# Kernel tuning notes

Measured on AMD Instinct MI355X. Metric: run time of the kernel, lower is better.

Reference implementation:

```python
import jax, jax.numpy as jnp
import numpy as np

SIGMA = 1.0

def setup_inputs() -> dict:
    key = jax.random.key(0)
    k1, k2 = jax.random.split(key)
    z = jax.random.normal(k1, (8192, 1024), dtype=jnp.float32)
    expert_keys = jax.random.normal(k2, (4096, 1024), dtype=jnp.float32)
    return {"z": z, "expert_keys": expert_keys}

def reference(z, expert_keys):
    # squared euclidean distances [N, E] = |z|^2 + |e|^2 - 2 z.e
    z_sq = jnp.sum(z * z, axis=-1, keepdims=True)          # [N, 1]
    e_sq = jnp.sum(expert_keys * expert_keys, axis=-1)     # [E]
    dist2 = z_sq + e_sq[None, :] - 2.0 * (z @ expert_keys.T)
    dist2 = jnp.maximum(dist2, 0.0)
    similarity = jnp.exp(-dist2 / (2.0 * SIGMA ** 2))       # [N, E]
    weights = jax.nn.softmax(similarity, axis=-1)            # [N, E]
    weighted_expert = weights @ expert_keys                  # [N, D]
    return (similarity, weighted_expert)
```

## Files before the change

kernel.cpp:

```cpp
#include <hip/hip_runtime.h>
#include <stdint.h>


#define M_TOK 8192
#define N_EXP 4096
#define D_DIM 1024

typedef __attribute__((ext_vector_type(4))) float f32x4;
typedef __attribute__((ext_vector_type(8))) short short8;
typedef unsigned short u16;
typedef unsigned int u32;

__device__ __forceinline__ u16 f32_to_bf16(float f) {
  u32 u = __builtin_bit_cast(u32, f);
  u += 0x7fff + ((u >> 16) & 1);
  return (u16)(u >> 16);
}

__device__ __forceinline__ void async16(const void* g, void* l) {
  __builtin_amdgcn_global_load_lds((__attribute__((address_space(1))) void*)(g),
                                   (__attribute__((address_space(3))) void*)(l),
                                   16, 0, 0);
}

__global__ __launch_bounds__(256) void prep_convert2(const float* __restrict__ zsrc,
                                                     const float* __restrict__ esrc,
                                                     u16* __restrict__ zdst,
                                                     u16* __restrict__ edst,
                                                     float* __restrict__ zsq,
                                                     float* __restrict__ esq) {
  int row = blockIdx.x;
  const float* src;
  u16* dst;
  float* sq;
  if (row < M_TOK) {
    src = zsrc + (size_t)row * D_DIM;
    dst = zdst + (size_t)row * D_DIM;
    sq = zsq + row;
  } else {
    int r = row - M_TOK;
    src = esrc + (size_t)r * D_DIM;
    dst = edst + (size_t)r * D_DIM;
    sq = esq + r;
  }
  int t = threadIdx.x;
  const float4 v = ((const float4*)src)[t];
  ushort4 h;
  h.x = f32_to_bf16(v.x); h.y = f32_to_bf16(v.y);
  h.z = f32_to_bf16(v.z); h.w = f32_to_bf16(v.w);
  ((ushort4*)dst)[t] = h;
  float p = v.x * v.x + v.y * v.y + v.z * v.z + v.w * v.w;
#pragma unroll
  for (int off = 1; off < 64; off <<= 1) p += __shfl_xor(p, off, 64);
  __shared__ float partial[4];
  if ((t & 63) == 0) partial[t >> 6] = p;
  __syncthreads();
  if (t == 0) *sq = partial[0] + partial[1] + partial[2] + partial[3];
}

__global__ __launch_bounds__(256) void transpose_bf16(const u16* __restrict__ src,
                                                      u16* __restrict__ dst) {
  __shared__ u16 tile[64][65];
  int e0 = blockIdx.x * 64;
  int d0 = blockIdx.y * 64;
  int t = threadIdx.x;
  int lr = t >> 4;
  int lc = (t & 15) * 4;
#pragma unroll
  for (int r8 = 0; r8 < 4; ++r8) {
    int row = lr + r8 * 16;
    ushort4 v = *(const ushort4*)(src + (size_t)(e0 + row) * D_DIM + d0 + lc);
    tile[row][lc + 0] = v.x; tile[row][lc + 1] = v.y;
    tile[row][lc + 2] = v.z; tile[row][lc + 3] = v.w;
  }
  __syncthreads();
#pragma unroll
  for (int r8 = 0; r8 < 4; ++r8) {
    int dl = lr + r8 * 16;
    ushort4 v;
    v.x = tile[lc + 0][dl]; v.y = tile[lc + 1][dl];
    v.z = tile[lc + 2][dl]; v.w = tile[lc + 3][dl];
    *(ushort4*)(dst + (size_t)(d0 + dl) * N_EXP + e0 + lc) = v;
  }
}

template <int EPI>
__global__ __launch_bounds__(256) void gemm_bt(const u16* __restrict__ A,
                                               const u16* __restrict__ Bt,
                                               int Mdim, int Ndim, int Kdim,
                                               float* __restrict__ out, int ldo,
                                               const float* __restrict__ a_sq,
                                               const float* __restrict__ b_sq,
                                               float* __restrict__ rowsum,
                                               u16* __restrict__ wb,
                                               const float* __restrict__ scale) {
  constexpr int BM = 128, BN = 128, BK = 64;
  __shared__ __align__(16) u16 smA[2 * BM * BK];
  __shared__ __align__(16) u16 smB[2 * BN * BK];

  const int nTilesN = Ndim / BN;
  const int nwg = (Mdim / BM) * nTilesN;
  const int cpx = nwg >> 3;
  const int wg = blockIdx.x;
  const int swz = (wg & 7) * cpx + (wg >> 3);
  const int m0 = (swz / nTilesN) * BM;
  const int n0 = (swz % nTilesN) * BN;

  const int t = threadIdx.x;
  const int l = t & 63;
  const int w = t >> 6;
  const int wr = w >> 1, wc = w & 1;

  const int lr8 = l >> 3;
  const int cswz = (((l & 7) ^ lr8) << 3);

  f32x4 acc[4][4];
#pragma unroll
  for (int i = 0; i < 4; ++i)
#pragma unroll
    for (int j = 0; j < 4; ++j) acc[i][j] = (f32x4){0.f, 0.f, 0.f, 0.f};

  const int nIter = Kdim / BK;

#pragma unroll
  for (int i = 0; i < 4; ++i) {
    int s = i * 4 + w;
    int row = s * 8 + lr8;
    async16(A + (size_t)(m0 + row) * Kdim + cswz, smA + s * 512);
    async16(Bt + (size_t)(n0 + row) * Kdim + cswz, smB + s * 512);
  }
  __syncthreads();

  int cur = 0;
  for (int it = 0; it < nIter; ++it) {
    if (it + 1 < nIter) {
      const int k0 = (it + 1) * BK;
      const int nb = (cur ^ 1) * 8192;
#pragma unroll
      for (int i = 0; i < 4; ++i) {
        int s = i * 4 + w;
        int row = s * 8 + lr8;
        async16(A + (size_t)(m0 + row) * Kdim + k0 + cswz, smA + nb + s * 512);
        async16(Bt + (size_t)(n0 + row) * Kdim + k0 + cswz, smB + nb + s * 512);
      }
    }

    const int cbase = cur * 8192;
#pragma unroll
    for (int ks = 0; ks < 2; ++ks) {
      short8 af[4], bf[4];
      const int lrow = l & 15;
      const int kb = ks * 64 + ((l >> 4) << 4);
#pragma unroll
      for (int mi = 0; mi < 4; ++mi) {
        int row = wr * 64 + mi * 16 + lrow;
        int addr = row * 128 + (kb ^ ((row & 7) << 4));
        af[mi] = *(const short8*)(smA + cbase + (addr >> 1));
      }
#pragma unroll
      for (int ni = 0; ni < 4; ++ni) {
        int row = wc * 64 + ni * 16 + lrow;
        int addr = row * 128 + (kb ^ ((row & 7) << 4));
        bf[ni] = *(const short8*)(smB + cbase + (addr >> 1));
      }
#pragma unroll
      for (int mi = 0; mi < 4; ++mi)
#pragma unroll
        for (int ni = 0; ni < 4; ++ni)
          acc[mi][ni] = __builtin_amdgcn_mfma_f32_16x16x32_bf16(
              bf[ni], af[mi], acc[mi][ni], 0, 0, 0);
    }

    __syncthreads();
    cur ^= 1;
  }

  const int lcol = l & 15;
  const int rgrp = l >> 4;
  if (EPI == 1) {
#pragma unroll
    for (int mi = 0; mi < 4; ++mi) {
      int grow = m0 + wr * 64 + mi * 16 + lcol;
      float zq = a_sq[grow];
      float esum = 0.f;
#pragma unroll
      for (int ni = 0; ni < 4; ++ni) {
        int ncol = n0 + wc * 64 + ni * 16 + rgrp * 4;
        f32x4 eqv = *(const f32x4*)(b_sq + ncol);
        f32x4 simv;
        ushort4 wv;
#pragma unroll
        for (int r = 0; r < 4; ++r) {
          float dist2 = fmaxf(zq + eqv[r] - 2.0f * acc[mi][ni][r], 0.0f);
          float sim = __expf(-0.5f * dist2);
          simv[r] = sim;
          float es = __expf(sim);
          (&wv.x)[r] = f32_to_bf16(es);
          esum += es;
        }
        *(f32x4*)(out + (size_t)grow * ldo + ncol) = simv;
        if (wb) *(ushort4*)(wb + (size_t)grow * ldo + ncol) = wv;
      }
      esum += __shfl_xor(esum, 16, 64);
      esum += __shfl_xor(esum, 32, 64);
      if (rgrp == 0) atomicAdd(&rowsum[grow], esum);
    }
  } else {
#pragma unroll
    for (int mi = 0; mi < 4; ++mi) {
      int grow = m0 + wr * 64 + mi * 16 + lcol;
      float s = scale ? (1.0f / scale[grow]) : 1.0f;
#pragma unroll
      for (int ni = 0; ni < 4; ++ni) {
        int ncol = n0 + wc * 64 + ni * 16 + rgrp * 4;
        f32x4 v = acc[mi][ni] * s;
        *(f32x4*)(out + (size_t)grow * ldo + ncol) = v;
      }
    }
  }
}

__global__ __launch_bounds__(256) void weights_kernel(const float* __restrict__ sim,
                                                      const float* __restrict__ rowsum,
                                                      u16* __restrict__ wb) {
  size_t i = ((size_t)blockIdx.x * 256 + threadIdx.x) * 8;
  int row = (int)(i >> 12);
  float inv = 1.0f / rowsum[row];
  float4 a = *(const float4*)(sim + i);
  float4 b = *(const float4*)(sim + i + 4);
  u32 w0 = (u32)f32_to_bf16(__expf(a.x) * inv) | ((u32)f32_to_bf16(__expf(a.y) * inv) << 16);
  u32 w1 = (u32)f32_to_bf16(__expf(a.z) * inv) | ((u32)f32_to_bf16(__expf(a.w) * inv) << 16);
  u32 w2 = (u32)f32_to_bf16(__expf(b.x) * inv) | ((u32)f32_to_bf16(__expf(b.y) * inv) << 16);
  u32 w3 = (u32)f32_to_bf16(__expf(b.z) * inv) | ((u32)f32_to_bf16(__expf(b.w) * inv) << 16);
  uint4 o; o.x = w0; o.y = w1; o.z = w2; o.w = w3;
  *(uint4*)(wb + i) = o;
}

extern "C" void kernel_launch(void* const* d_in, const int* in_sizes, int n_in,
                              void* d_out, int out_size, void* d_ws, size_t ws_size,
                              hipStream_t stream) {
  const float* z = (const float*)d_in[0];
  const float* e = (const float*)d_in[1];
  float* out = (float*)d_out;
  float* sim = out;
  float* wout = out + (size_t)M_TOK * N_EXP;

  char* ws = (char*)d_ws;
  const size_t MB = (size_t)1 << 20;
  const bool fused = ws_size >= 96 * MB + 80 * 1024;

  if (fused) {
    u16* zb  = (u16*)ws;
    u16* eb  = (u16*)(ws + 16 * MB);
    u16* ebT = (u16*)(ws + 24 * MB);
    u16* Wb  = (u16*)(ws + 32 * MB);
    float* z_sq   = (float*)(ws + 96 * MB);
    float* e_sq   = (float*)(ws + 96 * MB + 32768);
    float* rowsum = (float*)(ws + 96 * MB + 49152);

    prep_convert2<<<M_TOK + N_EXP, 256, 0, stream>>>(z, e, zb, eb, z_sq, e_sq);
    transpose_bf16<<<dim3(N_EXP / 64, D_DIM / 64), 256, 0, stream>>>(eb, ebT);
    (void)hipMemsetAsync(rowsum, 0, M_TOK * sizeof(float), stream);

    gemm_bt<1><<<(M_TOK / 128) * (N_EXP / 128), 256, 0, stream>>>(
        zb, eb, M_TOK, N_EXP, D_DIM, sim, N_EXP, z_sq, e_sq, rowsum, Wb, nullptr);

    gemm_bt<0><<<(M_TOK / 128) * (D_DIM / 128), 256, 0, stream>>>(
        Wb, ebT, M_TOK, D_DIM, N_EXP, wout, D_DIM, nullptr, nullptr, nullptr,
        nullptr, rowsum);
  } else {
    u16* Wb  = (u16*)ws;
    u16* zb  = (u16*)ws;
    u16* eb  = (u16*)(ws + 64 * MB);
    u16* ebT = (u16*)(ws + 72 * MB);
    float* z_sq   = (float*)(ws + 80 * MB);
    float* e_sq   = (float*)(ws + 80 * MB + 32768);
    float* rowsum = (float*)(ws + 80 * MB + 49152);

    prep_convert2<<<M_TOK + N_EXP, 256, 0, stream>>>(z, e, zb, eb, z_sq, e_sq);
    transpose_bf16<<<dim3(N_EXP / 64, D_DIM / 64), 256, 0, stream>>>(eb, ebT);
    (void)hipMemsetAsync(rowsum, 0, M_TOK * sizeof(float), stream);

    gemm_bt<1><<<(M_TOK / 128) * (N_EXP / 128), 256, 0, stream>>>(
        zb, eb, M_TOK, N_EXP, D_DIM, sim, N_EXP, z_sq, e_sq, rowsum, nullptr, nullptr);

    weights_kernel<<<(M_TOK * (size_t)N_EXP) / (8 * 256), 256, 0, stream>>>(sim, rowsum, Wb);

    gemm_bt<0><<<(M_TOK / 128) * (D_DIM / 128), 256, 0, stream>>>(
        Wb, ebT, M_TOK, D_DIM, N_EXP, wout, D_DIM, nullptr, nullptr, nullptr,
        nullptr, nullptr);
  }
}
```

Baseline: 201.1 us.

## Replace similarity GEMM with 256x256-tile 8-wave pipelined kernel

Adds a new kernel for the distance/similarity GEMM that uses 256x256 tiles and 512 threads (8 waves). It interleaves LDS fragment loads, async global-to-LDS staging and MFMA quarters, separated by explicit barriers, waitcnts and setprio. The goal is more data reuse per tile and global load latency hidden behind MFMA work. The cost is higher register and LDS pressure (128KB LDS per block) and fewer workgroups (512) to spread across CUs. Only the fused workspace path is switched; the fallback path keeps the old kernel.

```diff
diff --git a/kernel.cpp b/kernel.cpp
--- a/kernel.cpp
+++ b/kernel.cpp
@@ -84,6 +84,175 @@
   }
 }
 
+__device__ __forceinline__ short8 lds_frag(const u16* base, int rh, int kbyte) {
+  int ab = rh * 128 + (kbyte ^ ((rh & 7) << 4));
+  return *(const short8*)((const char*)base + ab);
+}
+
+template <int MOFF, int NOFF>
+__device__ __forceinline__ void mfma_q(f32x4 (&acc)[8][4], short8 (&af)[4][2],
+                                       short8 (&bf)[4][2]) {
+#pragma unroll
+  for (int mi = 0; mi < 4; ++mi)
+#pragma unroll
+    for (int ni = 0; ni < 2; ++ni)
+#pragma unroll
+      for (int ks = 0; ks < 2; ++ks)
+        acc[MOFF + mi][NOFF + ni] = __builtin_amdgcn_mfma_f32_16x16x32_bf16(
+            bf[NOFF + ni][ks], af[mi][ks], acc[MOFF + mi][NOFF + ni], 0, 0, 0);
+}
+
+#define BAR() __builtin_amdgcn_s_barrier()
+#define WAIT_LGKM0() do { asm volatile("s_waitcnt lgkmcnt(0)" ::: "memory"); \
+                          __builtin_amdgcn_sched_barrier(0); } while (0)
+#define WAIT_VM(n) do { asm volatile("s_waitcnt vmcnt(" #n ")" ::: "memory"); \
+                        __builtin_amdgcn_sched_barrier(0); } while (0)
+
+__global__ __launch_bounds__(512, 2) void gemm8_sim(const u16* __restrict__ A,
+                                                    const u16* __restrict__ Bt,
+                                                    int Mdim, int Ndim, int Kdim,
+                                                    float* __restrict__ out, int ldo,
+                                                    const float* __restrict__ a_sq,
+                                                    const float* __restrict__ b_sq,
+                                                    float* __restrict__ rowsum,
+                                                    u16* __restrict__ wb) {
+  constexpr int BM = 256, BN = 256, BK = 64;
+  __shared__ __align__(16) u16 smA[2][2][8192];
+  __shared__ __align__(16) u16 smB[2][2][8192];
+
+  const int nTilesN = Ndim / BN;
+  const int nwg = (Mdim / BM) * nTilesN;
+  const int cpx = nwg >> 3;
+  const int wg = blockIdx.x;
+  const int swzb = (wg & 7) * cpx + (wg >> 3);
+  const int m0 = (swzb / nTilesN) * BM;
+  const int n0 = (swzb % nTilesN) * BN;
+
+  const int t = threadIdx.x;
+  const int l = t & 63;
+  const int wid = t >> 6;
+  const int wr = wid >> 2;
+  const int wc = wid & 3;
+  const int lrow = l & 15;
+  const int kb16 = (l >> 4) << 4;
+  const int lr8 = l >> 3;
+  const int cswz = ((l & 7) ^ lr8) << 3;
+  const int st_r0 = wid * 16 + lr8;
+  const int st_r1 = wid * 16 + 8 + lr8;
+  const int bhalf = wc >> 1;
+  const int brow0 = (wc & 1) * 64;
+
+#define STAGE_A8(bufp, half, kelem) do { \
+    async16(A + (size_t)(m0 + (half)*128 + st_r0) * Kdim + (kelem) + cswz, \
+            &smA[bufp][half][(wid*2 + 0) * 512]); \
+    async16(A + (size_t)(m0 + (half)*128 + st_r1) * Kdim + (kelem) + cswz, \
+            &smA[bufp][half][(wid*2 + 1) * 512]); } while (0)
+#define STAGE_B8(bufp, half, kelem) do { \
+    async16(Bt + (size_t)(n0 + (half)*128 + st_r0) * Kdim + (kelem) + cswz, \
+            &smB[bufp][half][(wid*2 + 0) * 512]); \
+    async16(Bt + (size_t)(n0 + (half)*128 + st_r1) * Kdim + (kelem) + cswz, \
+            &smB[bufp][half][(wid*2 + 1) * 512]); } while (0)
+
+  f32x4 acc[8][4];
+#pragma unroll
+  for (int i = 0; i < 8; ++i)
+#pragma unroll
+    for (int j = 0; j < 4; ++j) acc[i][j] = (f32x4){0.f, 0.f, 0.f, 0.f};
+
+  short8 af[4][2], bf[4][2];
+
+  STAGE_A8(0, 0, 0); STAGE_A8(0, 1, 0);
+  STAGE_B8(0, 0, 0); STAGE_B8(0, 1, 0);
+  STAGE_B8(1, 0, BK); STAGE_B8(1, 1, BK);
+  WAIT_VM(4);
+  BAR();
+
+#define DO_TILE8(u_, buf_, doA_, doB_, VMN_) do { \
+     \
+    _Pragma("unroll") for (int mi = 0; mi < 4; ++mi) { \
+      af[mi][0] = lds_frag(&smA[buf_][wr][0], mi*16 + lrow, kb16); \
+      af[mi][1] = lds_frag(&smA[buf_][wr][0], mi*16 + lrow, 64 + kb16); } \
+    _Pragma("unroll") for (int ni = 0; ni < 2; ++ni) { \
+      bf[ni][0] = lds_frag(&smB[buf_][bhalf][0], brow0 + ni*16 + lrow, kb16); \
+      bf[ni][1] = lds_frag(&smB[buf_][bhalf][0], brow0 + ni*16 + lrow, 64 + kb16); } \
+    if (doA_) STAGE_A8((buf_) ^ 1, 0, ((u_) + 1) * BK); \
+    BAR(); WAIT_LGKM0(); \
+    __builtin_amdgcn_s_setprio(1); \
+    mfma_q<0, 0>(acc, af, bf); \
+    __builtin_amdgcn_s_setprio(0); \
+    BAR(); \
+     \
+    _Pragma("unroll") for (int ni = 2; ni < 4; ++ni) { \
+      bf[ni][0] = lds_frag(&smB[buf_][bhalf][0], brow0 + ni*16 + lrow, kb16); \
+      bf[ni][1] = lds_frag(&smB[buf_][bhalf][0], brow0 + ni*16 + lrow, 64 + kb16); } \
+    if (doA_) STAGE_A8((buf_) ^ 1, 1, ((u_) + 1) * BK); \
+    BAR(); WAIT_LGKM0(); \
+    __builtin_amdgcn_s_setprio(1); \
+    mfma_q<0, 2>(acc, af, bf); \
+    __builtin_amdgcn_s_setprio(0); \
+    BAR(); \
+     \
+    _Pragma("unroll") for (int mi = 0; mi < 4; ++mi) { \
+      af[mi][0] = lds_frag(&smA[buf_][wr][0], (mi+4)*16 + lrow, kb16); \
+      af[mi][1] = lds_frag(&smA[buf_][wr][0], (mi+4)*16 + lrow, 64 + kb16); } \
+    if (doB_) STAGE_B8(buf_, 0, ((u_) + 2) * BK); \
+    BAR(); WAIT_LGKM0(); \
+    __builtin_amdgcn_s_setprio(1); \
+    mfma_q<4, 0>(acc, af, bf); \
+    __builtin_amdgcn_s_setprio(0); \
+    BAR(); \
+     \
+    if (doB_) STAGE_B8(buf_, 1, ((u_) + 2) * BK); \
+    BAR(); \
+    __builtin_amdgcn_s_setprio(1); \
+    mfma_q<4, 2>(acc, af, bf); \
+    __builtin_amdgcn_s_setprio(0); \
+    WAIT_VM(VMN_); \
+    BAR(); \
+  } while (0)
+
+  const int T = Kdim / BK;
+  for (int it = 0; it < T / 2 - 1; ++it) {
+    const int u0 = 2 * it;
+    DO_TILE8(u0, 0, true, true, 4);
+    DO_TILE8(u0 + 1, 1, true, true, 4);
+  }
+  DO_TILE8(T - 2, 0, true, false, 0);
+  DO_TILE8(T - 1, 1, false, false, 0);
+
+  const int rgrp = l >> 4;
+#pragma unroll
+  for (int mi = 0; mi < 8; ++mi) {
+    int grow = m0 + wr * 128 + mi * 16 + lrow;
+    float zq = a_sq[grow];
+    float esum = 0.f;
+#pragma unroll
+    for (int ni = 0; ni < 4; ++ni) {
+      int ncol = n0 + wc * 64 + ni * 16 + rgrp * 4;
+      f32x4 eqv = *(const f32x4*)(b_sq + ncol);
+      f32x4 simv;
+      ushort4 wv;
+#pragma unroll
+      for (int r = 0; r < 4; ++r) {
+        float dist2 = fmaxf(zq + eqv[r] - 2.0f * acc[mi][ni][r], 0.0f);
+        float sim = __expf(-0.5f * dist2);
+        simv[r] = sim;
+        float es = __expf(sim);
+        (&wv.x)[r] = f32_to_bf16(es);
+        esum += es;
+      }
+      *(f32x4*)(out + (size_t)grow * ldo + ncol) = simv;
+      *(ushort4*)(wb + (size_t)grow * ldo + ncol) = wv;
+    }
+    esum += __shfl_xor(esum, 16, 64);
+    esum += __shfl_xor(esum, 32, 64);
+    if (rgrp == 0) atomicAdd(&rowsum[grow], esum);
+  }
+#undef DO_TILE8
+#undef STAGE_A8
+#undef STAGE_B8
+}
+
 template <int EPI>
 __global__ __launch_bounds__(256) void gemm_bt(const u16* __restrict__ A,
                                                const u16* __restrict__ Bt,
@@ -110,7 +279,6 @@
   const int l = t & 63;
   const int w = t >> 6;
   const int wr = w >> 1, wc = w & 1;
-
   const int lr8 = l >> 3;
   const int cswz = (((l & 7) ^ lr8) << 3);
 
@@ -121,7 +289,6 @@
     for (int j = 0; j < 4; ++j) acc[i][j] = (f32x4){0.f, 0.f, 0.f, 0.f};
 
   const int nIter = Kdim / BK;
-
 #pragma unroll
   for (int i = 0; i < 4; ++i) {
     int s = i * 4 + w;
@@ -144,7 +311,6 @@
         async16(Bt + (size_t)(n0 + row) * Kdim + k0 + cswz, smB + nb + s * 512);
       }
     }
-
     const int cbase = cur * 8192;
 #pragma unroll
     for (int ks = 0; ks < 2; ++ks) {
@@ -170,7 +336,6 @@
           acc[mi][ni] = __builtin_amdgcn_mfma_f32_16x16x32_bf16(
               bf[ni], af[mi], acc[mi][ni], 0, 0, 0);
     }
-
     __syncthreads();
     cur ^= 1;
   }
@@ -262,8 +427,8 @@
     transpose_bf16<<<dim3(N_EXP / 64, D_DIM / 64), 256, 0, stream>>>(eb, ebT);
     (void)hipMemsetAsync(rowsum, 0, M_TOK * sizeof(float), stream);
 
-    gemm_bt<1><<<(M_TOK / 128) * (N_EXP / 128), 256, 0, stream>>>(
-        zb, eb, M_TOK, N_EXP, D_DIM, sim, N_EXP, z_sq, e_sq, rowsum, Wb, nullptr);
+    gemm8_sim<<<(M_TOK / 256) * (N_EXP / 256), 512, 0, stream>>>(
+        zb, eb, M_TOK, N_EXP, D_DIM, sim, N_EXP, z_sq, e_sq, rowsum, Wb);
 
     gemm_bt<0><<<(M_TOK / 128) * (D_DIM / 128), 256, 0, stream>>>(
         Wb, ebT, M_TOK, D_DIM, N_EXP, wout, D_DIM, nullptr, nullptr, nullptr,
```

Measured after the change: 191.2 us. 4.9% less time.

## Use 8-wave GEMM blocks and an LDS-transposed epilogue with coalesced row stores

Applied to the files above, without the earlier changes.

Each 128x128 GEMM block now runs 512 threads in a 2x4 wave grid, so each wave computes a 64x32 sub-tile. That halves the per-wave accumulators, and each thread issues fewer async global-to-LDS copies per stage. The intent is to raise the number of resident waves and hide latency better. In the similarity GEMM epilogue, results are staged through LDS so that each group of 8 lanes writes contiguous row segments. Those writes use nontemporal stores for the similarity output, plus the bf16 exp weights and per-row partial sums. The costs are reloading A fragments from LDS across more waves and issuing more rowsum atomics per row.

```diff
diff --git a/kernel.cpp b/kernel.cpp
--- a/kernel.cpp
+++ b/kernel.cpp
@@ -8,6 +8,7 @@
 
 typedef __attribute__((ext_vector_type(4))) float f32x4;
 typedef __attribute__((ext_vector_type(8))) short short8;
+typedef __attribute__((ext_vector_type(4))) unsigned short u16x4;
 typedef unsigned short u16;
 typedef unsigned int u32;
 
@@ -85,15 +86,15 @@
 }
 
 template <int EPI>
-__global__ __launch_bounds__(256) void gemm_bt(const u16* __restrict__ A,
-                                               const u16* __restrict__ Bt,
-                                               int Mdim, int Ndim, int Kdim,
-                                               float* __restrict__ out, int ldo,
-                                               const float* __restrict__ a_sq,
-                                               const float* __restrict__ b_sq,
-                                               float* __restrict__ rowsum,
-                                               u16* __restrict__ wb,
-                                               const float* __restrict__ scale) {
+__global__ __launch_bounds__(512, 4) void gemm_bt(const u16* __restrict__ A,
+                                                  const u16* __restrict__ Bt,
+                                                  int Mdim, int Ndim, int Kdim,
+                                                  float* __restrict__ out, int ldo,
+                                                  const float* __restrict__ a_sq,
+                                                  const float* __restrict__ b_sq,
+                                                  float* __restrict__ rowsum,
+                                                  u16* __restrict__ wb,
+                                                  const float* __restrict__ scale) {
   constexpr int BM = 128, BN = 128, BK = 64;
   __shared__ __align__(16) u16 smA[2 * BM * BK];
   __shared__ __align__(16) u16 smB[2 * BN * BK];
@@ -109,26 +110,24 @@
   const int t = threadIdx.x;
   const int l = t & 63;
   const int w = t >> 6;
-  const int wr = w >> 1, wc = w & 1;
-
+  const int wr = w >> 2;
+  const int wc = w & 3;
   const int lr8 = l >> 3;
   const int cswz = (((l & 7) ^ lr8) << 3);
-
-  f32x4 acc[4][4];
+  const int s0 = w * 2, s1 = w * 2 + 1;
+  const int str0 = s0 * 8 + lr8, str1 = s1 * 8 + lr8;
+
+  f32x4 acc[4][2];
 #pragma unroll
   for (int i = 0; i < 4; ++i)
 #pragma unroll
-    for (int j = 0; j < 4; ++j) acc[i][j] = (f32x4){0.f, 0.f, 0.f, 0.f};
+    for (int j = 0; j < 2; ++j) acc[i][j] = (f32x4){0.f, 0.f, 0.f, 0.f};
 
   const int nIter = Kdim / BK;
-
-#pragma unroll
-  for (int i = 0; i < 4; ++i) {
-    int s = i * 4 + w;
-    int row = s * 8 + lr8;
-    async16(A + (size_t)(m0 + row) * Kdim + cswz, smA + s * 512);
-    async16(Bt + (size_t)(n0 + row) * Kdim + cswz, smB + s * 512);
-  }
+  async16(A + (size_t)(m0 + str0) * Kdim + cswz, smA + s0 * 512);
+  async16(A + (size_t)(m0 + str1) * Kdim + cswz, smA + s1 * 512);
+  async16(Bt + (size_t)(n0 + str0) * Kdim + cswz, smB + s0 * 512);
+  async16(Bt + (size_t)(n0 + str1) * Kdim + cswz, smB + s1 * 512);
   __syncthreads();
 
   int cur = 0;
@@ -136,19 +135,15 @@
     if (it + 1 < nIter) {
       const int k0 = (it + 1) * BK;
       const int nb = (cur ^ 1) * 8192;
-#pragma unroll
-      for (int i = 0; i < 4; ++i) {
-        int s = i * 4 + w;
-        int row = s * 8 + lr8;
-        async16(A + (size_t)(m0 + row) * Kdim + k0 + cswz, smA + nb + s * 512);
-        async16(Bt + (size_t)(n0 + row) * Kdim + k0 + cswz, smB + nb + s * 512);
-      }
+      async16(A + (size_t)(m0 + str0) * Kdim + k0 + cswz, smA + nb + s0 * 512);
+      async16(A + (size_t)(m0 + str1) * Kdim + k0 + cswz, smA + nb + s1 * 512);
+      async16(Bt + (size_t)(n0 + str0) * Kdim + k0 + cswz, smB + nb + s0 * 512);
+      async16(Bt + (size_t)(n0 + str1) * Kdim + k0 + cswz, smB + nb + s1 * 512);
     }
-
     const int cbase = cur * 8192;
 #pragma unroll
     for (int ks = 0; ks < 2; ++ks) {
-      short8 af[4], bf[4];
+      short8 af[4], bf[2];
       const int lrow = l & 15;
       const int kb = ks * 64 + ((l >> 4) << 4);
 #pragma unroll
@@ -158,19 +153,18 @@
         af[mi] = *(const short8*)(smA + cbase + (addr >> 1));
       }
 #pragma unroll
-      for (int ni = 0; ni < 4; ++ni) {
-        int row = wc * 64 + ni * 16 + lrow;
+      for (int ni = 0; ni < 2; ++ni) {
+        int row = wc * 32 + ni * 16 + lrow;
         int addr = row * 128 + (kb ^ ((row & 7) << 4));
         bf[ni] = *(const short8*)(smB + cbase + (addr >> 1));
       }
 #pragma unroll
       for (int mi = 0; mi < 4; ++mi)
 #pragma unroll
-        for (int ni = 0; ni < 4; ++ni)
+        for (int ni = 0; ni < 2; ++ni)
           acc[mi][ni] = __builtin_amdgcn_mfma_f32_16x16x32_bf16(
               bf[ni], af[mi], acc[mi][ni], 0, 0, 0);
     }
-
     __syncthreads();
     cur ^= 1;
   }
@@ -178,32 +172,48 @@
   const int lcol = l & 15;
   const int rgrp = l >> 4;
   if (EPI == 1) {
+    float* ldsT = ((float*)smA) + w * (16 * 36);
+    const int rr = l >> 3;
+    const int c4 = (l & 7) * 4;
 #pragma unroll
     for (int mi = 0; mi < 4; ++mi) {
       int grow = m0 + wr * 64 + mi * 16 + lcol;
       float zq = a_sq[grow];
-      float esum = 0.f;
-#pragma unroll
-      for (int ni = 0; ni < 4; ++ni) {
-        int ncol = n0 + wc * 64 + ni * 16 + rgrp * 4;
+#pragma unroll
+      for (int ni = 0; ni < 2; ++ni) {
+        int ncol = n0 + wc * 32 + ni * 16 + rgrp * 4;
         f32x4 eqv = *(const f32x4*)(b_sq + ncol);
         f32x4 simv;
-        ushort4 wv;
 #pragma unroll
         for (int r = 0; r < 4; ++r) {
           float dist2 = fmaxf(zq + eqv[r] - 2.0f * acc[mi][ni][r], 0.0f);
-          float sim = __expf(-0.5f * dist2);
-          simv[r] = sim;
-          float es = __expf(sim);
-          (&wv.x)[r] = f32_to_bf16(es);
-          esum += es;
+          simv[r] = __expf(-0.5f * dist2);
         }
-        *(f32x4*)(out + (size_t)grow * ldo + ncol) = simv;
-        if (wb) *(ushort4*)(wb + (size_t)grow * ldo + ncol) = wv;
-      }
-      esum += __shfl_xor(esum, 16, 64);
-      esum += __shfl_xor(esum, 32, 64);
-      if (rgrp == 0) atomicAdd(&rowsum[grow], esum);
+        *(f32x4*)(ldsT + lcol * 36 + ni * 16 + rgrp * 4) = simv;
+      }
+      asm volatile("s_waitcnt lgkmcnt(0)" ::: "memory");
+#pragma unroll
+      for (int pass = 0; pass < 2; ++pass) {
+        int rrow = pass * 8 + rr;
+        f32x4 sv = *(const f32x4*)(ldsT + rrow * 36 + c4);
+        int growr = m0 + wr * 64 + mi * 16 + rrow;
+        size_t gbase = (size_t)growr * ldo + (n0 + wc * 32 + c4);
+        __builtin_nontemporal_store(sv, (f32x4*)(out + gbase));
+        f32x4 es;
+#pragma unroll
+        for (int r = 0; r < 4; ++r) es[r] = __expf(sv[r]);
+        if (wb) {
+          u16x4 wv;
+          wv.x = f32_to_bf16(es[0]); wv.y = f32_to_bf16(es[1]);
+          wv.z = f32_to_bf16(es[2]); wv.w = f32_to_bf16(es[3]);
+          *(u16x4*)(wb + gbase) = wv;
+        }
+        float p = es[0] + es[1] + es[2] + es[3];
+        p += __shfl_xor(p, 1, 64);
+        p += __shfl_xor(p, 2, 64);
+        p += __shfl_xor(p, 4, 64);
+        if ((l & 7) == 0) atomicAdd(&rowsum[growr], p);
+      }
     }
   } else {
 #pragma unroll
@@ -211,8 +221,8 @@
       int grow = m0 + wr * 64 + mi * 16 + lcol;
       float s = scale ? (1.0f / scale[grow]) : 1.0f;
 #pragma unroll
-      for (int ni = 0; ni < 4; ++ni) {
-        int ncol = n0 + wc * 64 + ni * 16 + rgrp * 4;
+      for (int ni = 0; ni < 2; ++ni) {
+        int ncol = n0 + wc * 32 + ni * 16 + rgrp * 4;
         f32x4 v = acc[mi][ni] * s;
         *(f32x4*)(out + (size_t)grow * ldo + ncol) = v;
       }
@@ -262,10 +272,10 @@
     transpose_bf16<<<dim3(N_EXP / 64, D_DIM / 64), 256, 0, stream>>>(eb, ebT);
     (void)hipMemsetAsync(rowsum, 0, M_TOK * sizeof(float), stream);
 
-    gemm_bt<1><<<(M_TOK / 128) * (N_EXP / 128), 256, 0, stream>>>(
+    gemm_bt<1><<<(M_TOK / 128) * (N_EXP / 128), 512, 0, stream>>>(
         zb, eb, M_TOK, N_EXP, D_DIM, sim, N_EXP, z_sq, e_sq, rowsum, Wb, nullptr);
 
-    gemm_bt<0><<<(M_TOK / 128) * (D_DIM / 128), 256, 0, stream>>>(
+    gemm_bt<0><<<(M_TOK / 128) * (D_DIM / 128), 512, 0, stream>>>(
         Wb, ebT, M_TOK, D_DIM, N_EXP, wout, D_DIM, nullptr, nullptr, nullptr,
         nullptr, rowsum);
   } else {
@@ -281,12 +291,12 @@
     transpose_bf16<<<dim3(N_EXP / 64, D_DIM / 64), 256, 0, stream>>>(eb, ebT);
     (void)hipMemsetAsync(rowsum, 0, M_TOK * sizeof(float), stream);
 
-    gemm_bt<1><<<(M_TOK / 128) * (N_EXP / 128), 256, 0, stream>>>(
+    gemm_bt<1><<<(M_TOK / 128) * (N_EXP / 128), 512, 0, stream>>>(
         zb, eb, M_TOK, N_EXP, D_DIM, sim, N_EXP, z_sq, e_sq, rowsum, nullptr, nullptr);
 
     weights_kernel<<<(M_TOK * (size_t)N_EXP) / (8 * 256), 256, 0, stream>>>(sim, rowsum, Wb);
 
-    gemm_bt<0><<<(M_TOK / 128) * (D_DIM / 128), 256, 0, stream>>>(
+    gemm_bt<0><<<(M_TOK / 128) * (D_DIM / 128), 512, 0, stream>>>(
         Wb, ebT, M_TOK, D_DIM, N_EXP, wout, D_DIM, nullptr, nullptr, nullptr,
         nullptr, nullptr);
   }
```

Measured after the change: 195.7 us. 2.7% less time.
